# Performance work log

Hardware: AMD Instinct MI355X
Metric: run time of the kernel (lower is better)

The kernel has to match this reference:

```python
import jax, jax.numpy as jnp
import numpy as np

B, S, D, H = 2, 2048, 1024, 16
DK = D // H
FF_HIDDEN = 2048  # FeedForward default hidden_dim (fixed, not 4*D)


def setup_inputs() -> dict:
    key = jax.random.key(0)
    ks = jax.random.split(key, 16)
    s = 0.02
    inp = {
        "query": jax.random.normal(ks[0], (B, S, D), jnp.float32),
        "key": jax.random.normal(ks[1], (B, S, D), jnp.float32),
        "value": jax.random.normal(ks[2], (B, S, D), jnp.float32),
        "Wq": jax.random.normal(ks[3], (D, D), jnp.float32) * s,
        "bq": jnp.zeros((D,), jnp.float32),
        "Wk": jax.random.normal(ks[4], (D, D), jnp.float32) * s,
        "bk": jnp.zeros((D,), jnp.float32),
        "Wv": jax.random.normal(ks[5], (D, D), jnp.float32) * s,
        "bv": jnp.zeros((D,), jnp.float32),
        "ln_g": jnp.ones((D,), jnp.float32),
        "ln_b": jnp.zeros((D,), jnp.float32),
        "W1": jax.random.normal(ks[6], (D, FF_HIDDEN), jnp.float32) * s,
        "b1": jnp.zeros((FF_HIDDEN,), jnp.float32),
        "W2": jax.random.normal(ks[7], (FF_HIDDEN, D), jnp.float32) * s,
        "b2": jnp.zeros((D,), jnp.float32),
    }
    return inp


def reference(query, key, value, Wq, bq, Wk, bk, Wv, bv, ln_g, ln_b, W1, b1, W2, b2):
    # QKV projections
    q = query @ Wq + bq  # [B,S,D]
    k = key @ Wk + bk
    v = value @ Wv + bv
    # split heads -> [B,H,S,DK]
    q = q.reshape(B, S, H, DK).transpose(0, 2, 1, 3)
    k = k.reshape(B, S, H, DK).transpose(0, 2, 1, 3)
    v = v.reshape(B, S, H, DK).transpose(0, 2, 1, 3)
    # naive attention: full [B,H,S,S] scores (faithful to source)
    scores = jnp.einsum("bhqd,bhkd->bhqk", q, k) / jnp.sqrt(jnp.float32(DK))
    probs = jax.nn.softmax(scores, axis=-1)  # dropout = identity (eval)
    attn = jnp.einsum("bhqk,bhkd->bhqd", probs, v)
    attn = attn.transpose(0, 2, 1, 3).reshape(B, S, D)
    # LayerNorm
    mu = attn.mean(axis=-1, keepdims=True)
    var = attn.var(axis=-1, keepdims=True)
    ffi = (attn - mu) / jnp.sqrt(var + 1e-5) * ln_g + ln_b
    # FeedForward (dropout = identity in eval)
    h = jax.nn.relu(ffi @ W1 + b1)
    ff = h @ W2 + b2
    return ffi + ff
```

## Files before the change

### kernel.cpp

```cpp
#include <hip/hip_runtime.h>
#include <hip/hip_bf16.h>


#define S_LEN 2048
#define DMODEL 1024
#define NROWS 4096
#define QSCALE (0.125f * 1.4426950408889634f)

typedef __attribute__((ext_vector_type(8))) short short8_t;
typedef __attribute__((ext_vector_type(4))) float f32x4;

__device__ __forceinline__ unsigned short f2bf(float f){
  union { float f; unsigned int u; } a; a.f = f;
  unsigned int r = a.u + 0x7fffu + ((a.u >> 16) & 1u);
  return (unsigned short)(r >> 16);
}
__device__ __forceinline__ unsigned int pack2(float lo, float hi){
  return (unsigned int)f2bf(lo) | ((unsigned int)f2bf(hi) << 16);
}
__device__ __forceinline__ float bf2f(unsigned short u){
  union { unsigned int u; float f; } a; a.u = ((unsigned int)u) << 16;
  return a.f;
}
__device__ __forceinline__ unsigned int cvtpk(float lo, float hi){
  unsigned int r;
  asm("v_cvt_pk_bf16_f32 %0, %1, %2" : "=v"(r) : "v"(lo), "v"(hi));
  return r;
}
__device__ __forceinline__ void gload_lds16(const void* g, void* l){
  __builtin_amdgcn_global_load_lds((const __attribute__((address_space(1))) unsigned int*)g,
                                   (__attribute__((address_space(3))) unsigned int*)l, 16, 0, 0);
}

__device__ __forceinline__ void tc_body(const float* __restrict__ in,
    unsigned short* __restrict__ out, int R, int C, int bx, int by){
  __shared__ __align__(16) unsigned short tile[64*76];
  int c0 = bx * 64, r0 = by * 64;
  int t = threadIdx.x;
#pragma unroll
  for (int i = 0; i < 4; i++){
    int slot = i*256 + t;
    int r = slot >> 4, c4 = slot & 15;
    float4 v = *(const float4*)(in + (size_t)(r0 + r)*C + c0 + c4*4);
    ushort4 u; u.x = f2bf(v.x); u.y = f2bf(v.y); u.z = f2bf(v.z); u.w = f2bf(v.w);
    *(ushort4*)&tile[r*76 + c4*4] = u;
  }
  __syncthreads();
#pragma unroll
  for (int i = 0; i < 4; i++){
    int slot = i*256 + t;
    int oc = slot >> 4, seg = slot & 15;
    ushort4 u;
    u.x = tile[(seg*4+0)*76 + oc];
    u.y = tile[(seg*4+1)*76 + oc];
    u.z = tile[(seg*4+2)*76 + oc];
    u.w = tile[(seg*4+3)*76 + oc];
    *(ushort4*)(out + (size_t)(c0 + oc)*R + r0 + seg*4) = u;
  }
}

__global__ __launch_bounds__(256) void prep_kernel(
    const float* __restrict__ q, const float* __restrict__ k, const float* __restrict__ v,
    const float* __restrict__ Wq, const float* __restrict__ Wk, const float* __restrict__ Wv,
    const float* __restrict__ W1, const float* __restrict__ W2,
    const float* __restrict__ bq, const float* __restrict__ bk, const float* __restrict__ bv,
    unsigned short* __restrict__ qx, unsigned short* __restrict__ WqkvT,
    unsigned short* __restrict__ W1T, unsigned short* __restrict__ W2T,
    float* __restrict__ biascat)
{
  int bid = blockIdx.x;
  if (bid < 6144){
    const float* src = bid < 2048 ? q : (bid < 4096 ? k : v);
    int sub = bid & 2047;
    size_t i = (size_t)(sub*256 + threadIdx.x) * 8;
    float4 a = *(const float4*)(src + i);
    float4 b = *(const float4*)(src + i + 4);
    uint4 u; u.x = pack2(a.x,a.y); u.y = pack2(a.z,a.w); u.z = pack2(b.x,b.y); u.w = pack2(b.z,b.w);
    *(uint4*)(qx + (size_t)(bid >> 11)*4194304 + i) = u;
  } else if (bid < 6912){
    int sub = bid - 6144;
    int z = sub >> 8;
    const float* in = z == 0 ? Wq : (z == 1 ? Wk : Wv);
    tc_body(in, WqkvT + (size_t)z*1048576, 1024, 1024, sub & 15, (sub >> 4) & 15);
  } else if (bid < 7424){
    int sub = bid - 6912;
    tc_body(W1, W1T, 1024, 2048, sub & 31, sub >> 5);
  } else if (bid < 7936){
    int sub = bid - 7424;
    tc_body(W2, W2T, 2048, 1024, sub & 15, sub >> 4);
  } else {
    int i = (bid - 7936)*256 + threadIdx.x;
    biascat[i] = i < 1024 ? bq[i] : (i < 2048 ? bk[i-1024] : bv[i-2048]);
  }
}

template<bool OBF16, bool RELU, bool RESID, int NF, bool WV>
__global__ __launch_bounds__(256, 2) void gemm_bt(
    const unsigned short* __restrict__ A, const unsigned short* __restrict__ Bt,
    const float* __restrict__ bias, float scale, int scale_ncols, size_t aSel,
    unsigned short* __restrict__ Ob, float* __restrict__ Of,
    const unsigned short* __restrict__ resid, unsigned short* __restrict__ vtOut,
    int M, int N, int K)
{
  __shared__ __align__(16) unsigned short As[2*128*64];
  __shared__ __align__(16) unsigned short Bs[2*32*NF*64];
  char* AsB = (char*)As;
  char* BsB = (char*)Bs;
  int tid = threadIdx.x, lane = tid & 63, wave = tid >> 6;
  int wr = wave >> 1, wc = wave & 1;
  int m0 = blockIdx.y * 128, n0 = blockIdx.x * (32*NF);
  int qr = lane & 15, g = lane >> 4;
  f32x4 acc[4][NF];
#pragma unroll
  for (int i = 0; i < 4; i++)
#pragma unroll
    for (int j = 0; j < NF; j++) acc[i][j] = (f32x4){0.f,0.f,0.f,0.f};

  int lr = lane >> 3, ls = lane & 7;
  int scol = (ls ^ lr) * 8;
  const unsigned short* Ag = A + (size_t)(n0 >> 10)*aSel + (size_t)(m0 + wave*32 + lr)*K + scol;
  const unsigned short* Bg = Bt + (size_t)(n0 + wave*8*NF + lr)*K + scol;

  int rx = qr & 7;
  int aoff = (wr*64 + qr)*128 + ((g ^ rx) << 4);
  int boff = (wc*16*NF + qr)*128 + ((g ^ rx) << 4);

  int NT = K >> 6;
#pragma unroll
  for (int i = 0; i < 4; i++)
    gload_lds16(Ag + (size_t)i*8*K, AsB + wave*4096 + i*1024);
#pragma unroll
  for (int i = 0; i < NF; i++)
    gload_lds16(Bg + (size_t)i*8*K, BsB + wave*NF*1024 + i*1024);

  for (int it = 0; it < NT; ++it){
    int cur = it & 1;
    if (it + 1 < NT){
      int k1 = (it + 1) << 6;
      char* ad = AsB + (cur^1)*16384 + wave*4096;
      char* bd = BsB + (cur^1)*NF*4096 + wave*NF*1024;
#pragma unroll
      for (int i = 0; i < 4; i++)
        gload_lds16(Ag + (size_t)i*8*K + k1, ad + i*1024);
#pragma unroll
      for (int i = 0; i < NF; i++)
        gload_lds16(Bg + (size_t)i*8*K + k1, bd + i*1024);
      if constexpr (NF == 4) asm volatile("s_waitcnt vmcnt(8)" ::: "memory");
      else                   asm volatile("s_waitcnt vmcnt(6)" ::: "memory");
    } else {
      asm volatile("s_waitcnt vmcnt(0)" ::: "memory");
    }
    __builtin_amdgcn_s_barrier();
    asm volatile("" ::: "memory");

    const char* ka = AsB + cur*16384;
    const char* kb = BsB + cur*NF*4096;
    short8_t af[2][4], bfv[2][NF];
#pragma unroll
    for (int mi = 0; mi < 4; mi++){
      af[0][mi] = *(const short8_t*)(ka + aoff + mi*2048);
      af[1][mi] = *(const short8_t*)(ka + (aoff^64) + mi*2048);
    }
#pragma unroll
    for (int ni = 0; ni < NF; ni++){
      bfv[0][ni] = *(const short8_t*)(kb + boff + ni*2048);
      bfv[1][ni] = *(const short8_t*)(kb + (boff^64) + ni*2048);
    }
#pragma unroll
    for (int kh = 0; kh < 2; kh++)
#pragma unroll
      for (int mi = 0; mi < 4; mi++)
#pragma unroll
        for (int ni = 0; ni < NF; ni++)
          acc[mi][ni] = __builtin_amdgcn_mfma_f32_16x16x32_bf16(af[kh][mi], bfv[kh][ni], acc[mi][ni], 0, 0, 0);

    asm volatile("s_waitcnt lgkmcnt(0)" ::: "memory");
    __builtin_amdgcn_s_barrier();
    asm volatile("" ::: "memory");
  }

  bool vblock = WV && (n0 >= 2048);
#pragma unroll
  for (int ni = 0; ni < NF; ni++){
    int col = n0 + wc*16*NF + ni*16 + qr;
    float bs = bias[col];
    float sc = (col < scale_ncols) ? scale : 1.f;
#pragma unroll
    for (int mi = 0; mi < 4; mi++){
      int rowb = m0 + wr*64 + mi*16 + g*4;
      if (vblock){
        ushort4 uv;
        uv.x = f2bf(acc[mi][ni][0] + bs);
        uv.y = f2bf(acc[mi][ni][1] + bs);
        uv.z = f2bf(acc[mi][ni][2] + bs);
        uv.w = f2bf(acc[mi][ni][3] + bs);
        *(ushort4*)(vtOut + (size_t)(col - 2048)*4096 + rowb) = uv;
      } else {
#pragma unroll
        for (int r = 0; r < 4; r++){
          int row = rowb + r;
          float v = (acc[mi][ni][r] + bs) * sc;
          if constexpr (RELU) v = fmaxf(v, 0.f);
          if constexpr (RESID) v += bf2f(resid[(size_t)row*N + col]);
          if constexpr (OBF16) Ob[(size_t)row*N + col] = f2bf(v);
          else                 Of[(size_t)row*N + col] = v;
        }
      }
    }
  }
}

__global__ __launch_bounds__(256, 2) void flash_attn(
    const unsigned short* __restrict__ qkv,
    const unsigned short* __restrict__ vT,
    unsigned short* __restrict__ attn)
{
  __shared__ __align__(16) char smem[49152];
  int tid = threadIdx.x, lane = tid & 63, wave = tid >> 6;
  int bid = blockIdx.x;
  int orig = (bid & 7) * 64 + (bid >> 3);
  int bh = orig >> 4, qb = orig & 15;
  int b = bh >> 4, hd = bh & 15;
  int q0 = qb * 128 + wave * 32;
  int qr = lane & 15, g = lane >> 4;

  short8_t qf[2][2];
#pragma unroll
  for (int qg = 0; qg < 2; qg++){
    const unsigned short* qptr = qkv + (size_t)(b*S_LEN + q0 + 16*qg + qr)*3072 + hd*64 + g*8;
    qf[qg][0] = *(const short8_t*)qptr;
    qf[qg][1] = *(const short8_t*)(qptr + 32);
  }

  const f32x4 z4 = {0.f,0.f,0.f,0.f};
  f32x4 oacc[4][2];
#pragma unroll
  for (int tv = 0; tv < 4; tv++)
#pragma unroll
    for (int qg = 0; qg < 2; qg++) oacc[tv][qg] = z4;
  float lsum[2] = {0.f, 0.f};

  int lrow = lane >> 3, lslot = lane & 7;
  int sw = (lslot ^ lrow) * 8;
  const unsigned short* kg = qkv + 1024 + (size_t)(b*S_LEN + wave*8 + lrow)*3072 + hd*64 + sw;
  const unsigned short* vg = vT + (size_t)(hd*64 + wave*8 + lrow)*4096 + b*S_LEN + sw;

  int rx = qr & 7;
  int koff0 = qr*128 + ((g ^ rx) * 16);
  int koff1 = koff0 ^ 64;

  char* Pb = smem + 32768 + wave*4096;
  int gh = g >> 1;
  int pw0 = qr*128 + 8*(g & 1);
  int pr0 = qr*128;

  {
    char* kb_ = smem + wave*1024;
    char* vb_ = smem + 16384 + wave*1024;
    gload_lds16(kg,                       kb_);
    gload_lds16(kg + (size_t)32*3072,     kb_ + 4096);
    gload_lds16(vg,                       vb_);
    gload_lds16(vg + (size_t)32*4096,     vb_ + 4096);
  }

  int cur = 0;
  for (int it = 0; it < S_LEN/64; ++it){
    if (it + 1 < S_LEN/64){
      int kv1 = (it + 1) * 64;
      char* kb_ = smem + (cur^1)*8192 + wave*1024;
      char* vb_ = smem + 16384 + (cur^1)*8192 + wave*1024;
      gload_lds16(kg + (size_t)kv1*3072,        kb_);
      gload_lds16(kg + (size_t)(kv1+32)*3072,   kb_ + 4096);
      gload_lds16(vg + kv1,                     vb_);
      gload_lds16(vg + (size_t)32*4096 + kv1,   vb_ + 4096);
      asm volatile("s_waitcnt vmcnt(4)" ::: "memory");
    } else {
      asm volatile("s_waitcnt vmcnt(0)" ::: "memory");
    }
    __builtin_amdgcn_s_barrier();
    asm volatile("" ::: "memory");

    const char* kb = smem + cur*8192;
    const char* vb = smem + 16384 + cur*8192;

    f32x4 st[4][2];
    __builtin_amdgcn_s_setprio(1);
#pragma unroll
    for (int t = 0; t < 4; t++){
      short8_t kf0 = *(const short8_t*)(kb + koff0 + t*2048);
      short8_t kf1 = *(const short8_t*)(kb + koff1 + t*2048);
#pragma unroll
      for (int qg = 0; qg < 2; qg++){
        st[t][qg] = __builtin_amdgcn_mfma_f32_16x16x32_bf16(kf0, qf[qg][0], z4, 0, 0, 0);
        st[t][qg] = __builtin_amdgcn_mfma_f32_16x16x32_bf16(kf1, qf[qg][1], st[t][qg], 0, 0, 0);
      }
    }
    __builtin_amdgcn_s_setprio(0);

#pragma unroll
    for (int qg = 0; qg < 2; qg++){
      float ps0 = 0.f, ps1 = 0.f;
#pragma unroll
      for (int t = 0; t < 4; t++){
        float p0 = exp2f(st[t][qg][0]);
        float p1 = exp2f(st[t][qg][1]);
        float p2 = exp2f(st[t][qg][2]);
        float p3 = exp2f(st[t][qg][3]);
        uint2 wv; wv.x = cvtpk(p0, p1); wv.y = cvtpk(p2, p3);
        *(uint2*)(Pb + qg*2048 + pw0 + (((2*t + gh) ^ rx) << 4)) = wv;
        ps0 += p0 + p1;
        ps1 += p2 + p3;
      }
      lsum[qg] += ps0 + ps1;
    }

    short8_t pf[2][2];
#pragma unroll
    for (int qg = 0; qg < 2; qg++){
      pf[0][qg] = *(const short8_t*)(Pb + qg*2048 + pr0 + (((0 + g) ^ rx) << 4));
      pf[1][qg] = *(const short8_t*)(Pb + qg*2048 + pr0 + (((4 + g) ^ rx) << 4));
    }

    __builtin_amdgcn_s_setprio(1);
#pragma unroll
    for (int tv = 0; tv < 4; tv++){
      short8_t vf0 = *(const short8_t*)(vb + koff0 + tv*2048);
      short8_t vf1 = *(const short8_t*)(vb + koff1 + tv*2048);
#pragma unroll
      for (int qg = 0; qg < 2; qg++){
        oacc[tv][qg] = __builtin_amdgcn_mfma_f32_16x16x32_bf16(vf0, pf[0][qg], oacc[tv][qg], 0, 0, 0);
        oacc[tv][qg] = __builtin_amdgcn_mfma_f32_16x16x32_bf16(vf1, pf[1][qg], oacc[tv][qg], 0, 0, 0);
      }
    }
    __builtin_amdgcn_s_setprio(0);

    asm volatile("s_waitcnt lgkmcnt(0)" ::: "memory");
    __builtin_amdgcn_s_barrier();
    asm volatile("" ::: "memory");
    cur ^= 1;
  }
  float inv[2];
#pragma unroll
  for (int qg = 0; qg < 2; qg++){
    float l = lsum[qg];
    l += __shfl_xor(l, 16, 64);
    l += __shfl_xor(l, 32, 64);
    inv[qg] = 1.f / l;
  }

  __syncthreads();
  float* ot = (float*)(smem + wave*8320);
#pragma unroll
  for (int qg = 0; qg < 2; qg++)
#pragma unroll
    for (int tv = 0; tv < 4; tv++)
#pragma unroll
      for (int r = 0; r < 4; r++)
        ot[(qg*16 + qr)*65 + tv*16 + g*4 + r] = oacc[tv][qg][r] * inv[qg];
  __syncthreads();
  int seg = lane & 3;
#pragma unroll
  for (int rr = 0; rr < 2; rr++){
    int row = rr*16 + (lane >> 2);
    const float* src = ot + row*65 + seg*16;
    unsigned short* dst = attn + (size_t)(b*S_LEN + qb*128 + wave*32 + row)*DMODEL + hd*64 + seg*16;
    uint4 u0, u1;
    u0.x = pack2(src[0],  src[1]);  u0.y = pack2(src[2],  src[3]);
    u0.z = pack2(src[4],  src[5]);  u0.w = pack2(src[6],  src[7]);
    u1.x = pack2(src[8],  src[9]);  u1.y = pack2(src[10], src[11]);
    u1.z = pack2(src[12], src[13]); u1.w = pack2(src[14], src[15]);
    *(uint4*)dst       = u0;
    *(uint4*)(dst + 8) = u1;
  }
}

__global__ __launch_bounds__(256) void layernorm_kernel(const unsigned short* __restrict__ x,
    const float* __restrict__ gw, const float* __restrict__ bw,
    unsigned short* __restrict__ yb)
{
  int row = blockIdx.x, t = threadIdx.x;
  uint2 raw = *(const uint2*)(x + (size_t)row*DMODEL + t*4);
  float4 v;
  v.x = bf2f((unsigned short)(raw.x & 0xffff));
  v.y = bf2f((unsigned short)(raw.x >> 16));
  v.z = bf2f((unsigned short)(raw.y & 0xffff));
  v.w = bf2f((unsigned short)(raw.y >> 16));
  float s = (v.x + v.y) + (v.z + v.w);
  float q = (v.x*v.x + v.y*v.y) + (v.z*v.z + v.w*v.w);
#pragma unroll
  for (int off = 1; off < 64; off <<= 1){
    s += __shfl_xor(s, off, 64);
    q += __shfl_xor(q, off, 64);
  }
  __shared__ float red[8];
  if ((t & 63) == 0){ red[(t >> 6)*2] = s; red[(t >> 6)*2 + 1] = q; }
  __syncthreads();
  s = red[0] + red[2] + red[4] + red[6];
  q = red[1] + red[3] + red[5] + red[7];
  float mu = s * (1.f/DMODEL);
  float var = q * (1.f/DMODEL) - mu*mu;
  float rstd = rsqrtf(var + 1e-5f);
  float4 gg = *(const float4*)(gw + t*4);
  float4 bb = *(const float4*)(bw + t*4);
  float4 o;
  o.x = (v.x - mu)*rstd*gg.x + bb.x;
  o.y = (v.y - mu)*rstd*gg.y + bb.y;
  o.z = (v.z - mu)*rstd*gg.z + bb.z;
  o.w = (v.w - mu)*rstd*gg.w + bb.w;
  uint2 u; u.x = pack2(o.x, o.y); u.y = pack2(o.z, o.w);
  *(uint2*)(yb + (size_t)row*DMODEL + t*4) = u;
}

extern "C" void kernel_launch(void* const* d_in, const int* in_sizes, int n_in,
                              void* d_out, int out_size, void* d_ws, size_t ws_size,
                              hipStream_t stream)
{
  const float* query = (const float*)d_in[0];
  const float* key_  = (const float*)d_in[1];
  const float* value = (const float*)d_in[2];
  const float* Wq = (const float*)d_in[3];
  const float* bq = (const float*)d_in[4];
  const float* Wk = (const float*)d_in[5];
  const float* bk = (const float*)d_in[6];
  const float* Wv = (const float*)d_in[7];
  const float* bv = (const float*)d_in[8];
  const float* ln_g = (const float*)d_in[9];
  const float* ln_b = (const float*)d_in[10];
  const float* W1 = (const float*)d_in[11];
  const float* b1 = (const float*)d_in[12];
  const float* W2 = (const float*)d_in[13];
  const float* b2 = (const float*)d_in[14];

  char* ws = (char*)d_ws;
  unsigned short* qx     = (unsigned short*)(ws + 0);
  unsigned short* WqkvT  = (unsigned short*)(ws + 25165824);
  unsigned short* W1T    = (unsigned short*)(ws + 31457280);
  unsigned short* W2T    = (unsigned short*)(ws + 35651584);
  unsigned short* qkvbuf = (unsigned short*)(ws + 39845888);
  unsigned short* vTb    = (unsigned short*)(ws + 65011712);
  unsigned short* attnb  = (unsigned short*)(ws + 73400320);
  unsigned short* hbuf   = (unsigned short*)(ws + 73400320);
  float*          biascat= (float*)(ws + 73400320 + 8388608);
  unsigned short* ffib   = (unsigned short*)(ws + 106954752);

  prep_kernel<<<7948, 256, 0, stream>>>(query, key_, value, Wq, Wk, Wv, W1, W2,
                                        bq, bk, bv, qx, WqkvT, W1T, W2T, biascat);

  gemm_bt<true,false,false,4,true><<<dim3(24,32), 256, 0, stream>>>(
      qx, WqkvT, biascat, QSCALE, 1024, (size_t)4194304,
      qkvbuf, nullptr, nullptr, vTb, 4096, 3072, 1024);
  flash_attn<<<512, 256, 0, stream>>>(qkvbuf, vTb, attnb);
  layernorm_kernel<<<4096, 256, 0, stream>>>(attnb, ln_g, ln_b, ffib);
  gemm_bt<true,true,false,4,false><<<dim3(16,32), 256, 0, stream>>>(
      ffib, W1T, b1, 1.f, 0, (size_t)0,
      hbuf, nullptr, nullptr, nullptr, 4096, 2048, 1024);
  gemm_bt<false,false,true,2,false><<<dim3(16,32), 256, 0, stream>>>(
      hbuf, W2T, b2, 1.f, 0, (size_t)0,
      nullptr, (float*)d_out, ffib, nullptr, 4096, 1024, 2048);
}
```

Before: 182.3 us.

## Split attention KV range in two and merge partials in layernorm

The flash attention grid is doubled so each block handles only half of the key/value sequence. Each block writes unnormalized fp32 partial outputs and per-row softmax sums to workspace, and the layernorm kernel adds the two partials and divides by the combined sum before normalizing. The aim is more blocks and shorter per-block loops, for better load balance and latency hiding. The cost is extra global traffic from fp32 partial buffers that are written and read back, instead of a single bf16 attention output.

```diff
diff --git a/kernel.cpp b/kernel.cpp
--- a/kernel.cpp
+++ b/kernel.cpp
@@ -213,13 +213,16 @@
 __global__ __launch_bounds__(256, 2) void flash_attn(
     const unsigned short* __restrict__ qkv,
     const unsigned short* __restrict__ vT,
-    unsigned short* __restrict__ attn)
+    float* __restrict__ Opart,
+    float* __restrict__ Lpart)
 {
   __shared__ __align__(16) char smem[49152];
   int tid = threadIdx.x, lane = tid & 63, wave = tid >> 6;
   int bid = blockIdx.x;
-  int orig = (bid & 7) * 64 + (bid >> 3);
-  int bh = orig >> 4, qb = orig & 15;
+  int orig = (bid & 7) * 128 + (bid >> 3);
+  int half = orig >> 9;
+  int rest = orig & 511;
+  int bh = rest >> 4, qb = rest & 15;
   int b = bh >> 4, hd = bh & 15;
   int q0 = qb * 128 + wave * 32;
   int qr = lane & 15, g = lane >> 4;
@@ -242,8 +245,10 @@
 
   int lrow = lane >> 3, lslot = lane & 7;
   int sw = (lslot ^ lrow) * 8;
-  const unsigned short* kg = qkv + 1024 + (size_t)(b*S_LEN + wave*8 + lrow)*3072 + hd*64 + sw;
-  const unsigned short* vg = vT + (size_t)(hd*64 + wave*8 + lrow)*4096 + b*S_LEN + sw;
+  const unsigned short* kg = qkv + 1024 +
+      (size_t)(b*S_LEN + half*1024 + wave*8 + lrow)*3072 + hd*64 + sw;
+  const unsigned short* vg = vT + (size_t)(hd*64 + wave*8 + lrow)*4096
+      + b*S_LEN + half*1024 + sw;
 
   int rx = qr & 7;
   int koff0 = qr*128 + ((g ^ rx) * 16);
@@ -264,8 +269,9 @@
   }
 
   int cur = 0;
-  for (int it = 0; it < S_LEN/64; ++it){
-    if (it + 1 < S_LEN/64){
+  const int NIT = 1024/64;
+  for (int it = 0; it < NIT; ++it){
+    if (it + 1 < NIT){
       int kv1 = (it + 1) * 64;
       char* kb_ = smem + (cur^1)*8192 + wave*1024;
       char* vb_ = smem + 16384 + (cur^1)*8192 + wave*1024;
@@ -339,13 +345,17 @@
     asm volatile("" ::: "memory");
     cur ^= 1;
   }
-  float inv[2];
 #pragma unroll
   for (int qg = 0; qg < 2; qg++){
-    float l = lsum[qg];
-    l += __shfl_xor(l, 16, 64);
-    l += __shfl_xor(l, 32, 64);
-    inv[qg] = 1.f / l;
+    lsum[qg] += __shfl_xor(lsum[qg], 16, 64);
+    lsum[qg] += __shfl_xor(lsum[qg], 32, 64);
+  }
+  if (g == 0){
+#pragma unroll
+    for (int qg = 0; qg < 2; qg++){
+      int row = b*S_LEN + q0 + 16*qg + qr;
+      Lpart[(size_t)half*65536 + row*16 + hd] = lsum[qg];
+    }
   }
 
   __syncthreads();
@@ -356,35 +366,39 @@
     for (int tv = 0; tv < 4; tv++)
 #pragma unroll
       for (int r = 0; r < 4; r++)
-        ot[(qg*16 + qr)*65 + tv*16 + g*4 + r] = oacc[tv][qg][r] * inv[qg];
+        ot[(qg*16 + qr)*65 + tv*16 + g*4 + r] = oacc[tv][qg][r];
   __syncthreads();
   int seg = lane & 3;
+  float* Obase = Opart + (size_t)half*4194304;
 #pragma unroll
   for (int rr = 0; rr < 2; rr++){
     int row = rr*16 + (lane >> 2);
     const float* src = ot + row*65 + seg*16;
-    unsigned short* dst = attn + (size_t)(b*S_LEN + qb*128 + wave*32 + row)*DMODEL + hd*64 + seg*16;
-    uint4 u0, u1;
-    u0.x = pack2(src[0],  src[1]);  u0.y = pack2(src[2],  src[3]);
-    u0.z = pack2(src[4],  src[5]);  u0.w = pack2(src[6],  src[7]);
-    u1.x = pack2(src[8],  src[9]);  u1.y = pack2(src[10], src[11]);
-    u1.z = pack2(src[12], src[13]); u1.w = pack2(src[14], src[15]);
-    *(uint4*)dst       = u0;
-    *(uint4*)(dst + 8) = u1;
-  }
-}
-
-__global__ __launch_bounds__(256) void layernorm_kernel(const unsigned short* __restrict__ x,
+    float* dst = Obase + (size_t)(b*S_LEN + qb*128 + wave*32 + row)*DMODEL + hd*64 + seg*16;
+#pragma unroll
+    for (int i = 0; i < 4; i++){
+      float4 v; v.x = src[i*4]; v.y = src[i*4+1]; v.z = src[i*4+2]; v.w = src[i*4+3];
+      *(float4*)(dst + i*4) = v;
+    }
+  }
+}
+
+__global__ __launch_bounds__(256) void layernorm_kernel(
+    const float* __restrict__ Op, const float* __restrict__ Lp,
     const float* __restrict__ gw, const float* __restrict__ bw,
     unsigned short* __restrict__ yb)
 {
   int row = blockIdx.x, t = threadIdx.x;
-  uint2 raw = *(const uint2*)(x + (size_t)row*DMODEL + t*4);
+  int h = t >> 4;
+  float l = Lp[row*16 + h] + Lp[65536 + row*16 + h];
+  float inv = 1.f / l;
+  float4 o1 = *(const float4*)(Op + (size_t)row*DMODEL + t*4);
+  float4 o2 = *(const float4*)(Op + 4194304 + (size_t)row*DMODEL + t*4);
   float4 v;
-  v.x = bf2f((unsigned short)(raw.x & 0xffff));
-  v.y = bf2f((unsigned short)(raw.x >> 16));
-  v.z = bf2f((unsigned short)(raw.y & 0xffff));
-  v.w = bf2f((unsigned short)(raw.y >> 16));
+  v.x = (o1.x + o2.x) * inv;
+  v.y = (o1.y + o2.y) * inv;
+  v.z = (o1.z + o2.z) * inv;
+  v.w = (o1.w + o2.w) * inv;
   float s = (v.x + v.y) + (v.z + v.w);
   float q = (v.x*v.x + v.y*v.y) + (v.z*v.z + v.w*v.w);
 #pragma unroll
@@ -434,11 +448,12 @@
   char* ws = (char*)d_ws;
   unsigned short* qx     = (unsigned short*)(ws + 0);
   unsigned short* WqkvT  = (unsigned short*)(ws + 25165824);
+  float*          Lpart  = (float*)(ws + 25165824);
   unsigned short* W1T    = (unsigned short*)(ws + 31457280);
   unsigned short* W2T    = (unsigned short*)(ws + 35651584);
   unsigned short* qkvbuf = (unsigned short*)(ws + 39845888);
   unsigned short* vTb    = (unsigned short*)(ws + 65011712);
-  unsigned short* attnb  = (unsigned short*)(ws + 73400320);
+  float*          Opart  = (float*)(ws + 73400320);
   unsigned short* hbuf   = (unsigned short*)(ws + 73400320);
   float*          biascat= (float*)(ws + 73400320 + 8388608);
   unsigned short* ffib   = (unsigned short*)(ws + 106954752);
@@ -449,8 +464,8 @@
   gemm_bt<true,false,false,4,true><<<dim3(24,32), 256, 0, stream>>>(
       qx, WqkvT, biascat, QSCALE, 1024, (size_t)4194304,
       qkvbuf, nullptr, nullptr, vTb, 4096, 3072, 1024);
-  flash_attn<<<512, 256, 0, stream>>>(qkvbuf, vTb, attnb);
-  layernorm_kernel<<<4096, 256, 0, stream>>>(attnb, ln_g, ln_b, ffib);
+  flash_attn<<<1024, 256, 0, stream>>>(qkvbuf, vTb, Opart, Lpart);
+  layernorm_kernel<<<4096, 256, 0, stream>>>(Opart, Lpart, ln_g, ln_b, ffib);
   gemm_bt<true,true,false,4,false><<<dim3(16,32), 256, 0, stream>>>(
       ffib, W1T, b1, 1.f, 0, (size_t)0,
       hbuf, nullptr, nullptr, nullptr, 4096, 2048, 1024);
```

Result: slower. 187.7 us (+3.0%).
